# Kernel tuning notes

Hardware: AMD Instinct MI355X
Metric: run time of the kernel (lower is better)

Reference implementation:

```python
import jax, jax.numpy as jnp
import numpy as np

Z, K, H, Y = 128, 256, 512, 4  # z_size, key_size, hidden_size, y_dim


def setup_inputs() -> dict:
    key = jax.random.key(0)
    ks = jax.random.split(key, 8)
    B, T, P = 512, 32, 32
    s = lambda k, shape, sc: (jax.random.normal(k, shape, jnp.float32) * sc)
    return {
        "x_seq": jax.random.normal(ks[0], (B, T, P, P), jnp.float32),
        "W_enc": s(ks[1], (P * P, Z), 0.03),
        "gamma": jnp.ones((Z,), jnp.float32),
        "beta": jnp.zeros((Z,), jnp.float32),
        "W_ih": s(ks[2], (4 * H, K + 1), 0.05),
        "W_hh": s(ks[3], (4 * H, H), 0.04),
        "b_ih": jnp.zeros((4 * H,), jnp.float32),
        "b_hh": jnp.zeros((4 * H,), jnp.float32),
        "W_key": s(ks[4], (K, H), 0.06),
        "b_key": jnp.zeros((K,), jnp.float32),
        "W_g": s(ks[5], (1, H), 0.06),
        "b_g": jnp.zeros((1,), jnp.float32),
        "conf_gain": jnp.ones((1,), jnp.float32),
        "conf_bias": jnp.zeros((1,), jnp.float32),
        "W_y": s(ks[6], (Y, H), 0.06),
        "b_y": jnp.zeros((Y,), jnp.float32),
    }


def _lstm_cell(x, h, c, W_ih, W_hh, b_ih, b_hh):
    # PyTorch gate order: i, f, g, o
    gates = x @ W_ih.T + b_ih + h @ W_hh.T + b_hh
    i, f, g, o = jnp.split(gates, 4, axis=-1)
    c = jax.nn.sigmoid(f) * c + jax.nn.sigmoid(i) * jnp.tanh(g)
    h = jax.nn.sigmoid(o) * jnp.tanh(c)
    return h, c


def _forward(x_seq, W_enc, gamma, beta, W_ih, W_hh, b_ih, b_hh,
             W_key, b_key, W_g, b_g, conf_gain, conf_bias, W_y, b_y):
    B, T, P, _ = x_seq.shape
    # encoder: flatten -> linear to z_size (stand-in for Encoder_mlp)
    z = x_seq.reshape(B, T, P * P) @ W_enc  # [B, T, Z]
    # context norm over the sequence dim (single task segment)
    mu = z.mean(axis=1, keepdims=True)
    sig = jnp.sqrt(z.var(axis=1, keepdims=True) + 1e-8)
    z = (z - mu) / sig * gamma + beta

    M = T + 1  # T+1 steps; final step feeds a zero z_t
    z_pad = jnp.concatenate([z, jnp.zeros((B, 1, Z), z.dtype)], axis=1)  # [B, M, Z]

    h0 = jnp.zeros((B, H), z.dtype)
    c0 = jnp.zeros((B, H), z.dtype)
    kr0 = jnp.zeros((B, K + 1), z.dtype)
    Mk0 = jnp.zeros((B, M, K), z.dtype)
    Mv0 = jnp.zeros((B, M, Z), z.dtype)

    def step(carry, t):
        h, c, key_r, M_k, M_v = carry
        z_t = jax.lax.dynamic_index_in_dim(z_pad, t, axis=1, keepdims=False)  # [B, Z]
        h, c = _lstm_cell(key_r, h, c, W_ih, W_hh, b_ih, b_hh)
        key_w = jax.nn.relu(h @ W_key.T + b_key)          # [B, K]
        g = jax.nn.sigmoid(h @ W_g.T + b_g)               # [B, 1]
        y_lin = h @ W_y.T + b_y                            # [B, Y]
        # attention read over valid memory slots j < t
        scores = jnp.einsum('bz,bmz->bm', z_t, M_v)        # [B, M]
        valid = (jnp.arange(M) < t)[None, :]
        w_k = jax.nn.softmax(jnp.where(valid, scores, -1e9), axis=1)
        c_k = jax.nn.sigmoid(scores * conf_gain + conf_bias)
        kv = jnp.concatenate([M_k, c_k[..., None]], axis=2)  # [B, M, K+1]
        attn = g * jnp.einsum('bm,bmd->bd', w_k, kv)          # [B, K+1]
        key_r_new = jnp.where(t == 0, jnp.zeros_like(attn), attn)
        # append to memory at slot t
        M_k = jax.lax.dynamic_update_slice_in_dim(M_k, key_w[:, None, :], t, axis=1)
        M_v = jax.lax.dynamic_update_slice_in_dim(M_v, z_t[:, None, :], t, axis=1)
        return (h, c, key_r_new, M_k, M_v), y_lin

    _, ys = jax.lax.scan(step, (h0, c0, kr0, Mk0, Mv0), jnp.arange(M))
    return ys[-1]  # y_pred_linear from final step, [B, Y]


def reference(x_seq, W_enc, gamma, beta, W_ih, W_hh, b_ih, b_hh,
              W_key, b_key, W_g, b_g, conf_gain, conf_bias, W_y, b_y):
    y_pred_linear = _forward(x_seq, W_enc, gamma, beta, W_ih, W_hh, b_ih, b_hh,
                             W_key, b_key, W_g, b_g, conf_gain, conf_bias, W_y, b_y)
    y_pred = jnp.argmax(y_pred_linear, axis=1)
    return y_pred_linear, y_pred
```

## Files before the change

kernel.cpp:

```cpp
#include <hip/hip_runtime.h>
#include <math.h>

typedef unsigned short ushort;
typedef unsigned int uint;
typedef __bf16 bf16x8 __attribute__((ext_vector_type(8)));
typedef float f32x4 __attribute__((ext_vector_type(4)));

#define ZS    128
#define KS    256
#define HS    512
#define BATCH 512
#define TT    32
#define MM    33
#define NB    2304
#define KPAD  800
#define HOFF  272
#define LDA   800

static __device__ __forceinline__ float sigf(float x) { return 1.f / (1.f + expf(-x)); }
static __device__ __forceinline__ float bf2f(ushort u) { return __uint_as_float((uint)u << 16); }

__global__ void prep_w(const float* __restrict__ W_ih, const float* __restrict__ W_hh,
                       const float* __restrict__ W_key, const float* __restrict__ b_ih,
                       const float* __restrict__ b_hh, const float* __restrict__ b_key,
                       const float* __restrict__ W_enc,
                       ushort* __restrict__ Whi, ushort* __restrict__ Wlo,
                       ushort* __restrict__ Behi, ushort* __restrict__ Belo,
                       float* __restrict__ biasN)
{
    int idx = blockIdx.x * 256 + threadIdx.x;
    if (idx < NB) {
        float bv;
        if (idx < 2048) { int j = idx >> 2, gi = idx & 3, r = gi * 512 + j; bv = b_ih[r] + b_hh[r]; }
        else bv = b_key[idx - 2048];
        biasN[idx] = bv;
    }
    if (idx < NB * KPAD) {
        int n = idx / KPAD, k = idx - n * KPAD;
        float v = 0.f;
        if (n < 2048) {
            int j = n >> 2, gi = n & 3, r = gi * 512 + j;
            if (k < 257) v = W_ih[r * 257 + k];
            else if (k >= HOFF && k < HOFF + 512) v = W_hh[r * 512 + (k - HOFF)];
        } else {
            if (k >= HOFF && k < HOFF + 512) v = W_key[(n - 2048) * 512 + (k - HOFF)];
        }
        uint u = __float_as_uint(v);
        Whi[idx] = (ushort)(u >> 16);
        float lo = v - __uint_as_float(u & 0xFFFF0000u);
        Wlo[idx] = (ushort)(__float_as_uint(lo) >> 16);
    } else if (idx < NB * KPAD + 128 * 1024) {
        int e = idx - NB * KPAD;
        int n = e >> 10, k = e & 1023;
        float v = W_enc[k * 128 + n];
        uint u = __float_as_uint(v);
        Behi[e] = (ushort)(u >> 16);
        float lo = v - __uint_as_float(u & 0xFFFF0000u);
        Belo[e] = (ushort)(__float_as_uint(lo) >> 16);
    }
}

template<int BN, int MODE, bool PRESPLIT>
__global__ __launch_bounds__(256, 4)
void gemm_mfma(const float* __restrict__ A,
               const ushort* __restrict__ Ahi, const ushort* __restrict__ Alo, int lda,
               const ushort* __restrict__ Bhi, const ushort* __restrict__ Blo, int ldb,
               int nslice,
               float* __restrict__ out,
               ushort* __restrict__ outHi, ushort* __restrict__ outLo,
               const float* __restrict__ biasN,
               float* __restrict__ cst, float* __restrict__ Mk, int step)
{
    constexpr int NI = BN / 32;
    constexpr int AHI = 0, ALO = 32 * 40, BHI = 64 * 40, BLO = 64 * 40 + BN * 40;
    constexpr int BUF = 64 * 40 + 2 * BN * 40;
    __shared__ ushort lds[2 * BUF];

    const int tid = threadIdx.x;
    const int bx = blockIdx.x, by = blockIdx.y;
    const int row0 = by * 32, n0 = bx * BN;
    const int l = tid & 63, w = tid >> 6, wm = w >> 1, wn = w & 1;
    const int lm = l & 15, kg = (l >> 4) << 3;

    f32x4 acc[NI];
    const f32x4 zero4 = {0.f, 0.f, 0.f, 0.f};
#pragma unroll
    for (int ni = 0; ni < NI; ni++) acc[ni] = zero4;

    float4 avf;
    uint4 avu;
    uint4 bhv[BN / 64], blv[BN / 64];

    auto LOADG = [&](int s) {
        const int k0 = s * 32;
        if (PRESPLIT) {
            int idx = tid & 127, r = idx >> 2, c = (idx & 3) << 3;
            const ushort* src = (tid < 128) ? Ahi : Alo;
            avu = *(const uint4*)(src + (size_t)(row0 + r) * lda + k0 + c);
        } else {
            int r = tid >> 3, c = (tid & 7) << 2;
            avf = *(const float4*)(A + (size_t)(row0 + r) * lda + k0 + c);
        }
#pragma unroll
        for (int i = 0; i < BN / 64; i++) {
            int idx = tid + 256 * i, r = idx >> 2, c = (idx & 3) << 3;
            bhv[i] = *(const uint4*)(Bhi + (size_t)(n0 + r) * ldb + k0 + c);
            blv[i] = *(const uint4*)(Blo + (size_t)(n0 + r) * ldb + k0 + c);
        }
    };
    auto STORE = [&](int buf) {
        ushort* L = lds + buf * BUF;
        if (PRESPLIT) {
            int idx = tid & 127, r = idx >> 2, c = (idx & 3) << 3;
            *(uint4*)&L[(tid < 128 ? AHI : ALO) + r * 40 + c] = avu;
        } else {
            int r = tid >> 3, c = (tid & 7) << 2;
            uint u0 = __float_as_uint(avf.x), u1 = __float_as_uint(avf.y);
            uint u2 = __float_as_uint(avf.z), u3 = __float_as_uint(avf.w);
            uint hp0 = (u1 & 0xFFFF0000u) | (u0 >> 16);
            uint hp1 = (u3 & 0xFFFF0000u) | (u2 >> 16);
            float l0 = avf.x - __uint_as_float(u0 & 0xFFFF0000u);
            float l1 = avf.y - __uint_as_float(u1 & 0xFFFF0000u);
            float l2 = avf.z - __uint_as_float(u2 & 0xFFFF0000u);
            float l3 = avf.w - __uint_as_float(u3 & 0xFFFF0000u);
            uint lp0 = (__float_as_uint(l1) & 0xFFFF0000u) | (__float_as_uint(l0) >> 16);
            uint lp1 = (__float_as_uint(l3) & 0xFFFF0000u) | (__float_as_uint(l2) >> 16);
            *(uint2*)&L[AHI + r * 40 + c] = make_uint2(hp0, hp1);
            *(uint2*)&L[ALO + r * 40 + c] = make_uint2(lp0, lp1);
        }
#pragma unroll
        for (int i = 0; i < BN / 64; i++) {
            int idx = tid + 256 * i, r = idx >> 2, c = (idx & 3) << 3;
            *(uint4*)&L[BHI + r * 40 + c] = bhv[i];
            *(uint4*)&L[BLO + r * 40 + c] = blv[i];
        }
    };

    LOADG(0);
    STORE(0);
    for (int s = 0; s < nslice; s++) {
        if (s + 1 < nslice) LOADG(s + 1);
        __syncthreads();
        const ushort* L = lds + (s & 1) * BUF;
        bf16x8 ah, alv, bh[NI], bl[NI];
        {
            int r = wm * 16 + lm;
            ah  = *(const bf16x8*)&L[AHI + r * 40 + kg];
            alv = *(const bf16x8*)&L[ALO + r * 40 + kg];
        }
#pragma unroll
        for (int ni = 0; ni < NI; ni++) {
            int r = wn * (BN / 2) + ni * 16 + lm;
            bh[ni] = *(const bf16x8*)&L[BHI + r * 40 + kg];
            bl[ni] = *(const bf16x8*)&L[BLO + r * 40 + kg];
        }
#pragma unroll
        for (int ni = 0; ni < NI; ni++) {
            acc[ni] = __builtin_amdgcn_mfma_f32_16x16x32_bf16(ah,  bh[ni], acc[ni], 0, 0, 0);
            acc[ni] = __builtin_amdgcn_mfma_f32_16x16x32_bf16(ah,  bl[ni], acc[ni], 0, 0, 0);
            acc[ni] = __builtin_amdgcn_mfma_f32_16x16x32_bf16(alv, bh[ni], acc[ni], 0, 0, 0);
        }
        if (s + 1 < nslice) STORE((s + 1) & 1);
    }

    const int crow = (l >> 4) << 2;
    if (MODE == 0) {
#pragma unroll
        for (int ni = 0; ni < NI; ni++)
#pragma unroll
            for (int r = 0; r < 4; r++) {
                int m = row0 + wm * 16 + crow + r;
                int z = n0 + wn * (BN / 2) + ni * 16 + lm;
                out[(size_t)(m >> 5) * (MM * ZS) + (m & 31) * ZS + z] = acc[ni][r];
            }
    } else if (bx < 32) {
        __syncthreads();
        float* epi = (float*)lds;
        float* ew = epi + w * 544;
#pragma unroll
        for (int ni = 0; ni < NI; ni++)
#pragma unroll
            for (int r = 0; r < 4; r++) {
                int ml = crow + r, nl = ni * 16 + lm;
                ew[ml * 34 + nl] = acc[ni][r] + biasN[n0 + wn * 32 + nl];
            }
        __syncthreads();
        int row = tid >> 3, jj8 = tid & 7;
        int b = row0 + row;
        int j0 = bx * 16 + jj8 * 2;
        float2 cold = *(float2*)&cst[(size_t)b * HS + j0];
        float cc[2] = {cold.x, cold.y}, hv[2];
#pragma unroll
        for (int i = 0; i < 2; i++) {
            int jj = jj8 * 2 + i;
            float p[4];
#pragma unroll
            for (int g = 0; g < 4; g++) {
                int n = jj * 4 + g;
                int wv = (row >> 4) * 2 + (n >> 5);
                p[g] = epi[wv * 544 + (row & 15) * 34 + (n & 31)];
            }
            float ig = sigf(p[0]), fg = sigf(p[1]), gg = tanhf(p[2]), og = sigf(p[3]);
            float cn = fg * cc[i] + ig * gg;
            hv[i] = og * tanhf(cn);
            cc[i] = cn;
        }
        *(float2*)&cst[(size_t)b * HS + j0] = make_float2(cc[0], cc[1]);
        uint u0 = __float_as_uint(hv[0]), u1 = __float_as_uint(hv[1]);
        uint hp = (u1 & 0xFFFF0000u) | (u0 >> 16);
        float l0 = hv[0] - __uint_as_float(u0 & 0xFFFF0000u);
        float l1 = hv[1] - __uint_as_float(u1 & 0xFFFF0000u);
        uint lp = (__float_as_uint(l1) & 0xFFFF0000u) | (__float_as_uint(l0) >> 16);
        *(uint*)&outHi[(size_t)b * LDA + HOFF + j0] = hp;
        *(uint*)&outLo[(size_t)b * LDA + HOFF + j0] = lp;
    } else if (step >= 1) {
#pragma unroll
        for (int ni = 0; ni < NI; ni++)
#pragma unroll
            for (int r = 0; r < 4; r++) {
                int b = row0 + wm * 16 + crow + r;
                int cg = n0 + wn * 32 + ni * 16 + lm;
                float v = fmaxf(acc[ni][r] + biasN[cg], 0.f);
                Mk[((size_t)(step - 1) * BATCH + b) * KS + (cg - 2048)] = v;
            }
    }
}

__global__ void norm_k(float* __restrict__ z_pad, const float* __restrict__ gamma,
                       const float* __restrict__ beta)
{
    int b = blockIdx.x, zc = threadIdx.x;
    float* zb = z_pad + (size_t)b * (MM * ZS);
    float s = 0.f, s2 = 0.f;
    for (int t = 0; t < TT; t++) { float v = zb[t * ZS + zc]; s += v; s2 += v * v; }
    float mu = s * (1.f / 32.f);
    float var = s2 * (1.f / 32.f) - mu * mu;
    float rstd = 1.f / sqrtf(var + 1e-8f);
    float ga = gamma[zc], be = beta[zc];
    for (int t = 0; t < TT; t++) {
        float v = zb[t * ZS + zc];
        zb[t * ZS + zc] = (v - mu) * rstd * ga + be;
    }
    zb[TT * ZS + zc] = 0.f;
}

__global__ __launch_bounds__(256)
void scores_k(const float* __restrict__ z_pad, const float* __restrict__ cg_p,
              const float* __restrict__ cb_p, float* __restrict__ watt,
              float* __restrict__ wc)
{
    __shared__ float zs[MM * 129];
    int b = blockIdx.x, tid = threadIdx.x;
    const float* zb = z_pad + (size_t)b * (MM * ZS);
    for (int i = tid; i < MM * ZS; i += 256) {
        int m = i >> 7, k = i & 127;
        zs[m * 129 + k] = zb[i];
    }
    __syncthreads();
    float cg = cg_p[0], cb = cb_p[0];
    int wid = tid >> 6, lane = tid & 63;
    for (int t = 1 + wid; t <= 32; t += 4) {
        int m = lane;
        float s = -3.0e38f;
        if (m < t) {
            const float* zt = &zs[t * 129];
            const float* zm = &zs[m * 129];
            float acc = 0.f;
#pragma unroll 8
            for (int k = 0; k < ZS; k++) acc += zt[k] * zm[k];
            s = acc;
        }
        float mx = s;
        for (int off = 1; off < 64; off <<= 1) mx = fmaxf(mx, __shfl_xor(mx, off));
        float e = (m < t) ? expf(s - mx) : 0.f;
        float sum = e;
        for (int off = 1; off < 64; off <<= 1) sum += __shfl_xor(sum, off);
        float w = e / sum;
        if (m < t) watt[(b * MM + t) * MM + m] = w;
        float p = (m < t) ? w * sigf(s * cg + cb) : 0.f;
        for (int off = 1; off < 64; off <<= 1) p += __shfl_xor(p, off);
        if (lane == 0) wc[b * MM + t] = p;
    }
}

__global__ __launch_bounds__(256)
void post_k(ushort* __restrict__ inpHi, ushort* __restrict__ inpLo,
            const float* __restrict__ W_g, const float* __restrict__ b_g,
            const float* __restrict__ watt, const float* __restrict__ wc,
            const float* __restrict__ Mk, int t)
{
    __shared__ float red[256];
    __shared__ float wts[32];
    __shared__ float gsh;
    int b = blockIdx.x, tid = threadIdx.x;
    ushort* rHi = inpHi + (size_t)b * LDA;
    ushort* rLo = inpLo + (size_t)b * LDA;
    float h1 = bf2f(rHi[HOFF + tid]) + bf2f(rLo[HOFF + tid]);
    float h2 = bf2f(rHi[HOFF + 256 + tid]) + bf2f(rLo[HOFF + 256 + tid]);
    red[tid] = h1 * W_g[tid] + h2 * W_g[tid + 256];
    if (tid < t) wts[tid] = watt[(b * MM + t) * MM + tid];
    __syncthreads();
    for (int s = 128; s > 0; s >>= 1) {
        if (tid < s) red[tid] += red[tid + s];
        __syncthreads();
    }
    if (tid == 0) gsh = sigf(red[0] + b_g[0]);
    __syncthreads();
    float g = gsh;
    float acc = 0.f;
    for (int m = 0; m < t; m++)
        acc += wts[m] * Mk[((size_t)m * BATCH + b) * KS + tid];
    float v = g * acc;
    uint u = __float_as_uint(v);
    rHi[tid] = (ushort)(u >> 16);
    float lo = v - __uint_as_float(u & 0xFFFF0000u);
    rLo[tid] = (ushort)(__float_as_uint(lo) >> 16);
    if (tid == 0) {
        float vc = g * wc[b * MM + t];
        uint uc = __float_as_uint(vc);
        rHi[256] = (ushort)(uc >> 16);
        float lc = vc - __uint_as_float(uc & 0xFFFF0000u);
        rLo[256] = (ushort)(__float_as_uint(lc) >> 16);
    }
}

__global__ void y_k(const ushort* __restrict__ inpHi, const ushort* __restrict__ inpLo,
                    const float* __restrict__ W_y, const float* __restrict__ b_y,
                    float* __restrict__ out)
{
    int b = blockIdx.x, lane = threadIdx.x;
    const ushort* hHi = inpHi + (size_t)b * LDA + HOFF;
    const ushort* hLo = inpLo + (size_t)b * LDA + HOFF;
    float a0 = 0, a1 = 0, a2 = 0, a3 = 0;
    for (int r = 0; r < 8; r++) {
        int k = lane + r * 64;
        float hv = bf2f(hHi[k]) + bf2f(hLo[k]);
        a0 += hv * W_y[k];
        a1 += hv * W_y[512 + k];
        a2 += hv * W_y[1024 + k];
        a3 += hv * W_y[1536 + k];
    }
    for (int off = 32; off > 0; off >>= 1) {
        a0 += __shfl_xor(a0, off);
        a1 += __shfl_xor(a1, off);
        a2 += __shfl_xor(a2, off);
        a3 += __shfl_xor(a3, off);
    }
    if (lane == 0) {
        float y0 = a0 + b_y[0], y1 = a1 + b_y[1], y2 = a2 + b_y[2], y3 = a3 + b_y[3];
        out[b * 4 + 0] = y0; out[b * 4 + 1] = y1; out[b * 4 + 2] = y2; out[b * 4 + 3] = y3;
        int best = 0; float bv = y0;
        if (y1 > bv) { bv = y1; best = 1; }
        if (y2 > bv) { bv = y2; best = 2; }
        if (y3 > bv) { bv = y3; best = 3; }
        out[2048 + b] = (float)best;
    }
}

extern "C" void kernel_launch(void* const* d_in, const int* in_sizes, int n_in,
                              void* d_out, int out_size, void* d_ws, size_t ws_size,
                              hipStream_t stream)
{
    const float* x_seq = (const float*)d_in[0];
    const float* W_enc = (const float*)d_in[1];
    const float* gamma = (const float*)d_in[2];
    const float* beta  = (const float*)d_in[3];
    const float* W_ih  = (const float*)d_in[4];
    const float* W_hh  = (const float*)d_in[5];
    const float* b_ih  = (const float*)d_in[6];
    const float* b_hh  = (const float*)d_in[7];
    const float* W_key = (const float*)d_in[8];
    const float* b_key = (const float*)d_in[9];
    const float* W_g   = (const float*)d_in[10];
    const float* b_g   = (const float*)d_in[11];
    const float* cgain = (const float*)d_in[12];
    const float* cbias = (const float*)d_in[13];
    const float* W_y   = (const float*)d_in[14];
    const float* b_y   = (const float*)d_in[15];

    float* ws    = (float*)d_ws;
    float* z_pad = ws;
    float* watt  = z_pad + 2162688;
    float* wcv   = watt + 557568;
    float* Mk    = wcv + 16896;
    float* biasN = Mk + 4194304;
    float* cst   = biasN + 2304;
    ushort* inpHi0 = (ushort*)(cst + 262144);
    ushort* inpLo0 = inpHi0 + 409600;
    ushort* inpHi1 = inpLo0 + 409600;
    ushort* inpLo1 = inpHi1 + 409600;
    ushort* Whi  = inpLo1 + 409600;
    ushort* Wlo  = Whi + NB * KPAD;
    ushort* Behi = Wlo + NB * KPAD;
    ushort* Belo = Behi + 131072;

    hipMemsetAsync(cst, 0, 262144 * sizeof(float) + 4 * 409600 * sizeof(ushort), stream);

    prep_w<<<(NB * KPAD + 131072 + 255) / 256, 256, 0, stream>>>(
        W_ih, W_hh, W_key, b_ih, b_hh, b_key, W_enc, Whi, Wlo, Behi, Belo, biasN);

    gemm_mfma<128, 0, false><<<dim3(1, 512), 256, 0, stream>>>(
        x_seq, nullptr, nullptr, 1024, Behi, Belo, 1024, 32,
        z_pad, nullptr, nullptr, nullptr, nullptr, nullptr, 0);
    norm_k<<<512, 128, 0, stream>>>(z_pad, gamma, beta);
    scores_k<<<512, 256, 0, stream>>>(z_pad, cgain, cbias, watt, wcv);

    for (int t = 0; t <= 32; t++) {
        ushort* inHiC = (t & 1) ? inpHi1 : inpHi0;
        ushort* inLoC = (t & 1) ? inpLo1 : inpLo0;
        ushort* inHiN = (t & 1) ? inpHi0 : inpHi1;
        ushort* inLoN = (t & 1) ? inpLo0 : inpLo1;
        gemm_mfma<64, 1, true><<<dim3(36, 16), 256, 0, stream>>>(
            nullptr, inHiC, inLoC, LDA, Whi, Wlo, KPAD, 25,
            nullptr, inHiN, inLoN, biasN, cst, Mk, t);
        if (t >= 1 && t <= 31)
            post_k<<<512, 256, 0, stream>>>(inHiN, inLoN, W_g, b_g, watt, wcv, Mk, t);
    }
    y_k<<<512, 64, 0, stream>>>((0 ? inpHi0 : inpHi1), (0 ? inpLo0 : inpLo1),
                                W_y, b_y, (float*)d_out);
}
```

Baseline: 1.016 ms.

## Split encoder GEMM K-dimension, swizzle recurrent GEMM blocks, double-register prefetch

The encoder GEMM is split along K into two halves via blockIdx.z, with the second half written into the Mk scratch buffer and summed in norm_k. This doubles the block count to fill the GPU. The recurrent GEMM uses a 1D grid with an XCD-style swizzle of block indices to improve cache locality. The main loop is unrolled by two with two register prefetch sets so global loads are issued two slices ahead, and encoder launch bounds are relaxed to 3 blocks per SM. The cost is more registers and an extra partial-sum buffer round trip.

```diff
diff --git a/kernel.cpp b/kernel.cpp
--- a/kernel.cpp
+++ b/kernel.cpp
@@ -60,8 +60,54 @@
     }
 }
 
+#define LOADG_M(s, avf_, avu_, bhv_, blv_) do {                                   \
+    const int k0 = (s) * 32;                                                      \
+    if (PRESPLIT) {                                                               \
+        int idx = tid & 127, r = idx >> 2, c = (idx & 3) << 3;                    \
+        const ushort* srcp = (tid < 128) ? Ahi : Alo;                             \
+        avu_ = *(const uint4*)(srcp + (size_t)(row0 + r) * lda + k0 + c);         \
+    } else {                                                                      \
+        int r = tid >> 3, c = (tid & 7) << 2;                                     \
+        avf_ = *(const float4*)(A + (size_t)(row0 + r) * lda + k0 + c);           \
+    }                                                                             \
+    _Pragma("unroll")                                                             \
+    for (int i = 0; i < BN / 64; i++) {                                           \
+        int idx2 = tid + 256 * i, r2 = idx2 >> 2, c2 = (idx2 & 3) << 3;           \
+        bhv_[i] = *(const uint4*)(Bhi + (size_t)(n0 + r2) * ldb + k0 + c2);       \
+        blv_[i] = *(const uint4*)(Blo + (size_t)(n0 + r2) * ldb + k0 + c2);       \
+    }                                                                             \
+} while (0)
+
+#define STORE_M(buf, avf_, avu_, bhv_, blv_) do {                                 \
+    ushort* Lw = lds + (buf) * BUF;                                               \
+    if (PRESPLIT) {                                                               \
+        int idx = tid & 127, r = idx >> 2, c = (idx & 3) << 3;                    \
+        *(uint4*)&Lw[(tid < 128 ? AHI : ALO) + r * 40 + c] = avu_;                \
+    } else {                                                                     \
+        int r = tid >> 3, c = (tid & 7) << 2;                                    \
+        uint u0 = __float_as_uint(avf_.x), u1 = __float_as_uint(avf_.y);          \
+        uint u2 = __float_as_uint(avf_.z), u3 = __float_as_uint(avf_.w);          \
+        uint hp0 = (u1 & 0xFFFF0000u) | (u0 >> 16);                               \
+        uint hp1 = (u3 & 0xFFFF0000u) | (u2 >> 16);                               \
+        float l0 = avf_.x - __uint_as_float(u0 & 0xFFFF0000u);                    \
+        float l1 = avf_.y - __uint_as_float(u1 & 0xFFFF0000u);                    \
+        float l2 = avf_.z - __uint_as_float(u2 & 0xFFFF0000u);                    \
+        float l3 = avf_.w - __uint_as_float(u3 & 0xFFFF0000u);                    \
+        uint lp0 = (__float_as_uint(l1) & 0xFFFF0000u) | (__float_as_uint(l0) >> 16); \
+        uint lp1 = (__float_as_uint(l3) & 0xFFFF0000u) | (__float_as_uint(l2) >> 16); \
+        *(uint2*)&Lw[AHI + r * 40 + c] = make_uint2(hp0, hp1);                    \
+        *(uint2*)&Lw[ALO + r * 40 + c] = make_uint2(lp0, lp1);                    \
+    }                                                                             \
+    _Pragma("unroll")                                                             \
+    for (int i = 0; i < BN / 64; i++) {                                           \
+        int idx3 = tid + 256 * i, r3 = idx3 >> 2, c3 = (idx3 & 3) << 3;           \
+        *(uint4*)&Lw[BHI + r3 * 40 + c3] = bhv_[i];                               \
+        *(uint4*)&Lw[BLO + r3 * 40 + c3] = blv_[i];                               \
+    }                                                                             \
+} while (0)
+
 template<int BN, int MODE, bool PRESPLIT>
-__global__ __launch_bounds__(256, 4)
+__global__ __launch_bounds__(256, (MODE == 0) ? 3 : 4)
 void gemm_mfma(const float* __restrict__ A,
                const ushort* __restrict__ Ahi, const ushort* __restrict__ Alo, int lda,
                const ushort* __restrict__ Bhi, const ushort* __restrict__ Blo, int ldb,
@@ -77,7 +123,18 @@
     __shared__ ushort lds[2 * BUF];
 
     const int tid = threadIdx.x;
-    const int bx = blockIdx.x, by = blockIdx.y;
+    int bx, by;
+    if (MODE == 1) {
+        int wg = blockIdx.x;
+        int swz = (wg & 7) * 72 + (wg >> 3);
+        bx = swz >> 4; by = swz & 15;
+    } else {
+        bx = blockIdx.x; by = blockIdx.y;
+        A   += (size_t)blockIdx.z * 512;
+        Bhi += (size_t)blockIdx.z * 512;
+        Blo += (size_t)blockIdx.z * 512;
+        if (blockIdx.z) out = Mk;
+    }
     const int row0 = by * 32, n0 = bx * BN;
     const int l = tid & 63, w = tid >> 6, wm = w >> 1, wn = w & 1;
     const int lm = l & 15, kg = (l >> 4) << 3;
@@ -87,60 +144,11 @@
 #pragma unroll
     for (int ni = 0; ni < NI; ni++) acc[ni] = zero4;
 
-    float4 avf;
-    uint4 avu;
-    uint4 bhv[BN / 64], blv[BN / 64];
-
-    auto LOADG = [&](int s) {
-        const int k0 = s * 32;
-        if (PRESPLIT) {
-            int idx = tid & 127, r = idx >> 2, c = (idx & 3) << 3;
-            const ushort* src = (tid < 128) ? Ahi : Alo;
-            avu = *(const uint4*)(src + (size_t)(row0 + r) * lda + k0 + c);
-        } else {
-            int r = tid >> 3, c = (tid & 7) << 2;
-            avf = *(const float4*)(A + (size_t)(row0 + r) * lda + k0 + c);
-        }
-#pragma unroll
-        for (int i = 0; i < BN / 64; i++) {
-            int idx = tid + 256 * i, r = idx >> 2, c = (idx & 3) << 3;
-            bhv[i] = *(const uint4*)(Bhi + (size_t)(n0 + r) * ldb + k0 + c);
-            blv[i] = *(const uint4*)(Blo + (size_t)(n0 + r) * ldb + k0 + c);
-        }
-    };
-    auto STORE = [&](int buf) {
-        ushort* L = lds + buf * BUF;
-        if (PRESPLIT) {
-            int idx = tid & 127, r = idx >> 2, c = (idx & 3) << 3;
-            *(uint4*)&L[(tid < 128 ? AHI : ALO) + r * 40 + c] = avu;
-        } else {
-            int r = tid >> 3, c = (tid & 7) << 2;
-            uint u0 = __float_as_uint(avf.x), u1 = __float_as_uint(avf.y);
-            uint u2 = __float_as_uint(avf.z), u3 = __float_as_uint(avf.w);
-            uint hp0 = (u1 & 0xFFFF0000u) | (u0 >> 16);
-            uint hp1 = (u3 & 0xFFFF0000u) | (u2 >> 16);
-            float l0 = avf.x - __uint_as_float(u0 & 0xFFFF0000u);
-            float l1 = avf.y - __uint_as_float(u1 & 0xFFFF0000u);
-            float l2 = avf.z - __uint_as_float(u2 & 0xFFFF0000u);
-            float l3 = avf.w - __uint_as_float(u3 & 0xFFFF0000u);
-            uint lp0 = (__float_as_uint(l1) & 0xFFFF0000u) | (__float_as_uint(l0) >> 16);
-            uint lp1 = (__float_as_uint(l3) & 0xFFFF0000u) | (__float_as_uint(l2) >> 16);
-            *(uint2*)&L[AHI + r * 40 + c] = make_uint2(hp0, hp1);
-            *(uint2*)&L[ALO + r * 40 + c] = make_uint2(lp0, lp1);
-        }
-#pragma unroll
-        for (int i = 0; i < BN / 64; i++) {
-            int idx = tid + 256 * i, r = idx >> 2, c = (idx & 3) << 3;
-            *(uint4*)&L[BHI + r * 40 + c] = bhv[i];
-            *(uint4*)&L[BLO + r * 40 + c] = blv[i];
-        }
-    };
-
-    LOADG(0);
-    STORE(0);
-    for (int s = 0; s < nslice; s++) {
-        if (s + 1 < nslice) LOADG(s + 1);
-        __syncthreads();
+    float4 avf0, avf1;
+    uint4 avu0, avu1;
+    uint4 bhv0[BN / 64], blv0[BN / 64], bhv1[BN / 64], blv1[BN / 64];
+
+    auto COMPUTE = [&](int s) {
         const ushort* L = lds + (s & 1) * BUF;
         bf16x8 ah, alv, bh[NI], bl[NI];
         {
@@ -160,7 +168,22 @@
             acc[ni] = __builtin_amdgcn_mfma_f32_16x16x32_bf16(ah,  bl[ni], acc[ni], 0, 0, 0);
             acc[ni] = __builtin_amdgcn_mfma_f32_16x16x32_bf16(alv, bh[ni], acc[ni], 0, 0, 0);
         }
-        if (s + 1 < nslice) STORE((s + 1) & 1);
+    };
+
+    LOADG_M(0, avf0, avu0, bhv0, blv0);
+    STORE_M(0, avf0, avu0, bhv0, blv0);
+    if (nslice > 1) LOADG_M(1, avf1, avu1, bhv1, blv1);
+    for (int s = 0; s < nslice; s += 2) {
+        if (s + 2 < nslice) LOADG_M(s + 2, avf0, avu0, bhv0, blv0);
+        __syncthreads();
+        COMPUTE(s);
+        if (s + 1 < nslice) STORE_M((s + 1) & 1, avf1, avu1, bhv1, blv1);
+        if (s + 3 < nslice) LOADG_M(s + 3, avf1, avu1, bhv1, blv1);
+        __syncthreads();
+        if (s + 1 < nslice) {
+            COMPUTE(s + 1);
+            if (s + 2 < nslice) STORE_M((s + 2) & 1, avf0, avu0, bhv0, blv0);
+        }
     }
 
     const int crow = (l >> 4) << 2;
@@ -226,13 +249,21 @@
     }
 }
 
-__global__ void norm_k(float* __restrict__ z_pad, const float* __restrict__ gamma,
-                       const float* __restrict__ beta)
+#undef LOADG_M
+#undef STORE_M
+
+__global__ void norm_k(float* __restrict__ z_pad, const float* __restrict__ z2,
+                       const float* __restrict__ gamma, const float* __restrict__ beta)
 {
     int b = blockIdx.x, zc = threadIdx.x;
     float* zb = z_pad + (size_t)b * (MM * ZS);
+    const float* zb2 = z2 + (size_t)b * (MM * ZS);
     float s = 0.f, s2 = 0.f;
-    for (int t = 0; t < TT; t++) { float v = zb[t * ZS + zc]; s += v; s2 += v * v; }
+    for (int t = 0; t < TT; t++) {
+        float v = zb[t * ZS + zc] + zb2[t * ZS + zc];
+        zb[t * ZS + zc] = v;
+        s += v; s2 += v * v;
+    }
     float mu = s * (1.f / 32.f);
     float var = s2 * (1.f / 32.f) - mu * mu;
     float rstd = 1.f / sqrtf(var + 1e-8f);
@@ -399,10 +430,10 @@
     prep_w<<<(NB * KPAD + 131072 + 255) / 256, 256, 0, stream>>>(
         W_ih, W_hh, W_key, b_ih, b_hh, b_key, W_enc, Whi, Wlo, Behi, Belo, biasN);
 
-    gemm_mfma<128, 0, false><<<dim3(1, 512), 256, 0, stream>>>(
-        x_seq, nullptr, nullptr, 1024, Behi, Belo, 1024, 32,
-        z_pad, nullptr, nullptr, nullptr, nullptr, nullptr, 0);
-    norm_k<<<512, 128, 0, stream>>>(z_pad, gamma, beta);
+    gemm_mfma<128, 0, false><<<dim3(1, 512, 2), 256, 0, stream>>>(
+        x_seq, nullptr, nullptr, 1024, Behi, Belo, 1024, 16,
+        z_pad, nullptr, nullptr, nullptr, nullptr, Mk, 0);
+    norm_k<<<512, 128, 0, stream>>>(z_pad, Mk, gamma, beta);
     scores_k<<<512, 256, 0, stream>>>(z_pad, cgain, cbias, watt, wcv);
 
     for (int t = 0; t <= 32; t++) {
@@ -410,7 +441,7 @@
         ushort* inLoC = (t & 1) ? inpLo1 : inpLo0;
         ushort* inHiN = (t & 1) ? inpHi0 : inpHi1;
         ushort* inLoN = (t & 1) ? inpLo0 : inpLo1;
-        gemm_mfma<64, 1, true><<<dim3(36, 16), 256, 0, stream>>>(
+        gemm_mfma<64, 1, true><<<dim3(576), 256, 0, stream>>>(
             nullptr, inHiC, inLoC, LDA, Whi, Wlo, KPAD, 25,
             nullptr, inHiN, inLoN, biasN, cst, Mk, t);
         if (t >= 1 && t <= 31)
```

New measurement: 1.058 ms. 4.2% more time.

## Split recurrent GEMM along K into two partials and fuse cell with attention

Applied to the files above, without the earlier changes.

The per-step recurrent GEMM now runs as 1152 workgroups: the K dimension is split into two halves (13 and 12 slices), each writing a separate partial result to P0/P1. Workgroup indices are swizzled and the occupancy hint is raised. The fused LSTM epilogue and key ReLU are moved out of the GEMM into a new cell_k kernel that sums the partials, applies the gates, writes Mk, and also performs the post_k gate and attention work, reusing h from shared memory and the fresh key from registers. The aim is more parallelism in the latency-bound step GEMM, paid for by extra global traffic for the partials.

```diff
diff --git a/kernel.cpp b/kernel.cpp
--- a/kernel.cpp
+++ b/kernel.cpp
@@ -61,15 +61,13 @@
 }
 
 template<int BN, int MODE, bool PRESPLIT>
-__global__ __launch_bounds__(256, 4)
+__global__ __launch_bounds__(256, (MODE == 1) ? 5 : 4)
 void gemm_mfma(const float* __restrict__ A,
                const ushort* __restrict__ Ahi, const ushort* __restrict__ Alo, int lda,
                const ushort* __restrict__ Bhi, const ushort* __restrict__ Blo, int ldb,
                int nslice,
                float* __restrict__ out,
-               ushort* __restrict__ outHi, ushort* __restrict__ outLo,
-               const float* __restrict__ biasN,
-               float* __restrict__ cst, float* __restrict__ Mk, int step)
+               float* __restrict__ out2)
 {
     constexpr int NI = BN / 32;
     constexpr int AHI = 0, ALO = 32 * 40, BHI = 64 * 40, BLO = 64 * 40 + BN * 40;
@@ -77,7 +75,20 @@
     __shared__ ushort lds[2 * BUF];
 
     const int tid = threadIdx.x;
-    const int bx = blockIdx.x, by = blockIdx.y;
+    int bx, by, kb, kc;
+    if (MODE == 1) {
+        int wg = blockIdx.x;
+        int swz = (wg & 7) * 144 + (wg >> 3);
+        int zz = swz / 576;
+        int r  = swz - zz * 576;
+        bx = r >> 4; by = r & 15;
+        kb = zz ? 13 : 0;
+        kc = zz ? 12 : 13;
+        if (zz) out = out2;
+    } else {
+        bx = blockIdx.x; by = blockIdx.y;
+        kb = 0; kc = nslice;
+    }
     const int row0 = by * 32, n0 = bx * BN;
     const int l = tid & 63, w = tid >> 6, wm = w >> 1, wn = w & 1;
     const int lm = l & 15, kg = (l >> 4) << 3;
@@ -91,8 +102,8 @@
     uint4 avu;
     uint4 bhv[BN / 64], blv[BN / 64];
 
-    auto LOADG = [&](int s) {
-        const int k0 = s * 32;
+    auto LOADG = [&](int a) {
+        const int k0 = a * 32;
         if (PRESPLIT) {
             int idx = tid & 127, r = idx >> 2, c = (idx & 3) << 3;
             const ushort* src = (tid < 128) ? Ahi : Alo;
@@ -135,13 +146,8 @@
             *(uint4*)&L[BLO + r * 40 + c] = blv[i];
         }
     };
-
-    LOADG(0);
-    STORE(0);
-    for (int s = 0; s < nslice; s++) {
-        if (s + 1 < nslice) LOADG(s + 1);
-        __syncthreads();
-        const ushort* L = lds + (s & 1) * BUF;
+    auto COMPUTE = [&](int buf) {
+        const ushort* L = lds + buf * BUF;
         bf16x8 ah, alv, bh[NI], bl[NI];
         {
             int r = wm * 16 + lm;
@@ -160,7 +166,15 @@
             acc[ni] = __builtin_amdgcn_mfma_f32_16x16x32_bf16(ah,  bl[ni], acc[ni], 0, 0, 0);
             acc[ni] = __builtin_amdgcn_mfma_f32_16x16x32_bf16(alv, bh[ni], acc[ni], 0, 0, 0);
         }
-        if (s + 1 < nslice) STORE((s + 1) & 1);
+    };
+
+    LOADG(kb);
+    STORE(0);
+    for (int s = 0; s < kc; s++) {
+        if (s + 1 < kc) LOADG(kb + s + 1);
+        __syncthreads();
+        COMPUTE(s & 1);
+        if (s + 1 < kc) STORE((s + 1) & 1);
     }
 
     const int crow = (l >> 4) << 2;
@@ -173,56 +187,84 @@
                 int z = n0 + wn * (BN / 2) + ni * 16 + lm;
                 out[(size_t)(m >> 5) * (MM * ZS) + (m & 31) * ZS + z] = acc[ni][r];
             }
-    } else if (bx < 32) {
-        __syncthreads();
-        float* epi = (float*)lds;
-        float* ew = epi + w * 544;
-#pragma unroll
-        for (int ni = 0; ni < NI; ni++)
-#pragma unroll
-            for (int r = 0; r < 4; r++) {
-                int ml = crow + r, nl = ni * 16 + lm;
-                ew[ml * 34 + nl] = acc[ni][r] + biasN[n0 + wn * 32 + nl];
-            }
-        __syncthreads();
-        int row = tid >> 3, jj8 = tid & 7;
-        int b = row0 + row;
-        int j0 = bx * 16 + jj8 * 2;
-        float2 cold = *(float2*)&cst[(size_t)b * HS + j0];
-        float cc[2] = {cold.x, cold.y}, hv[2];
-#pragma unroll
-        for (int i = 0; i < 2; i++) {
-            int jj = jj8 * 2 + i;
-            float p[4];
-#pragma unroll
-            for (int g = 0; g < 4; g++) {
-                int n = jj * 4 + g;
-                int wv = (row >> 4) * 2 + (n >> 5);
-                p[g] = epi[wv * 544 + (row & 15) * 34 + (n & 31)];
-            }
-            float ig = sigf(p[0]), fg = sigf(p[1]), gg = tanhf(p[2]), og = sigf(p[3]);
-            float cn = fg * cc[i] + ig * gg;
-            hv[i] = og * tanhf(cn);
-            cc[i] = cn;
-        }
-        *(float2*)&cst[(size_t)b * HS + j0] = make_float2(cc[0], cc[1]);
-        uint u0 = __float_as_uint(hv[0]), u1 = __float_as_uint(hv[1]);
-        uint hp = (u1 & 0xFFFF0000u) | (u0 >> 16);
-        float l0 = hv[0] - __uint_as_float(u0 & 0xFFFF0000u);
-        float l1 = hv[1] - __uint_as_float(u1 & 0xFFFF0000u);
-        uint lp = (__float_as_uint(l1) & 0xFFFF0000u) | (__float_as_uint(l0) >> 16);
-        *(uint*)&outHi[(size_t)b * LDA + HOFF + j0] = hp;
-        *(uint*)&outLo[(size_t)b * LDA + HOFF + j0] = lp;
-    } else if (step >= 1) {
+    } else {
 #pragma unroll
         for (int ni = 0; ni < NI; ni++)
 #pragma unroll
             for (int r = 0; r < 4; r++) {
                 int b = row0 + wm * 16 + crow + r;
-                int cg = n0 + wn * 32 + ni * 16 + lm;
-                float v = fmaxf(acc[ni][r] + biasN[cg], 0.f);
-                Mk[((size_t)(step - 1) * BATCH + b) * KS + (cg - 2048)] = v;
+                int n = n0 + wn * (BN / 2) + ni * 16 + lm;
+                out[(size_t)b * NB + n] = acc[ni][r];
             }
+    }
+}
+
+__global__ __launch_bounds__(256)
+void cell_k(const float* __restrict__ P0, const float* __restrict__ P1,
+            const float* __restrict__ biasN, float* __restrict__ cst,
+            ushort* __restrict__ outHi, ushort* __restrict__ outLo,
+            float* __restrict__ Mk,
+            const float* __restrict__ W_g, const float* __restrict__ b_g,
+            const float* __restrict__ watt, const float* __restrict__ wc,
+            int t)
+{
+    __shared__ float hsh[512];
+    __shared__ float red[256];
+    __shared__ float wts[32];
+    __shared__ float gsh;
+    int b = blockIdx.x, tid = threadIdx.x;
+    const float* p0 = P0 + (size_t)b * NB;
+    const float* p1 = P1 + (size_t)b * NB;
+    ushort* rHi = outHi + (size_t)b * LDA;
+    ushort* rLo = outLo + (size_t)b * LDA;
+#pragma unroll
+    for (int u = 0; u < 2; u++) {
+        int j = tid + u * 256;
+        float4 a  = *(const float4*)(p0 + 4 * j);
+        float4 c4 = *(const float4*)(p1 + 4 * j);
+        float4 bb = *(const float4*)(biasN + 4 * j);
+        float gi = a.x + c4.x + bb.x;
+        float gf = a.y + c4.y + bb.y;
+        float gg = a.z + c4.z + bb.z;
+        float go = a.w + c4.w + bb.w;
+        float iv = sigf(gi), fv = sigf(gf), gv = tanhf(gg), ov = sigf(go);
+        float cn = fv * cst[(size_t)b * HS + j] + iv * gv;
+        float hv = ov * tanhf(cn);
+        cst[(size_t)b * HS + j] = cn;
+        hsh[j] = hv;
+        uint uu = __float_as_uint(hv);
+        rHi[HOFF + j] = (ushort)(uu >> 16);
+        float lo = hv - __uint_as_float(uu & 0xFFFF0000u);
+        rLo[HOFF + j] = (ushort)(__float_as_uint(lo) >> 16);
+    }
+    float kv = fmaxf(p0[2048 + tid] + p1[2048 + tid] + biasN[2048 + tid], 0.f);
+    if (t >= 1) Mk[((size_t)(t - 1) * BATCH + b) * KS + tid] = kv;
+    if (t < 1 || t > 31) return;
+    if (tid < t) wts[tid] = watt[(b * MM + t) * MM + tid];
+    __syncthreads();
+    red[tid] = hsh[tid] * W_g[tid] + hsh[tid + 256] * W_g[tid + 256];
+    __syncthreads();
+    for (int s = 128; s > 0; s >>= 1) {
+        if (tid < s) red[tid] += red[tid + s];
+        __syncthreads();
+    }
+    if (tid == 0) gsh = sigf(red[0] + b_g[0]);
+    __syncthreads();
+    float g = gsh;
+    float acc = wts[t - 1] * kv;
+    for (int m = 0; m < t - 1; m++)
+        acc += wts[m] * Mk[((size_t)m * BATCH + b) * KS + tid];
+    float v = g * acc;
+    uint u2 = __float_as_uint(v);
+    rHi[tid] = (ushort)(u2 >> 16);
+    float lo2 = v - __uint_as_float(u2 & 0xFFFF0000u);
+    rLo[tid] = (ushort)(__float_as_uint(lo2) >> 16);
+    if (tid == 0) {
+        float vc = g * wc[b * MM + t];
+        uint uc = __float_as_uint(vc);
+        rHi[256] = (ushort)(uc >> 16);
+        float lc = vc - __uint_as_float(uc & 0xFFFF0000u);
+        rLo[256] = (ushort)(__float_as_uint(lc) >> 16);
     }
 }
 
@@ -280,47 +322,6 @@
         float p = (m < t) ? w * sigf(s * cg + cb) : 0.f;
         for (int off = 1; off < 64; off <<= 1) p += __shfl_xor(p, off);
         if (lane == 0) wc[b * MM + t] = p;
-    }
-}
-
-__global__ __launch_bounds__(256)
-void post_k(ushort* __restrict__ inpHi, ushort* __restrict__ inpLo,
-            const float* __restrict__ W_g, const float* __restrict__ b_g,
-            const float* __restrict__ watt, const float* __restrict__ wc,
-            const float* __restrict__ Mk, int t)
-{
-    __shared__ float red[256];
-    __shared__ float wts[32];
-    __shared__ float gsh;
-    int b = blockIdx.x, tid = threadIdx.x;
-    ushort* rHi = inpHi + (size_t)b * LDA;
-    ushort* rLo = inpLo + (size_t)b * LDA;
-    float h1 = bf2f(rHi[HOFF + tid]) + bf2f(rLo[HOFF + tid]);
-    float h2 = bf2f(rHi[HOFF + 256 + tid]) + bf2f(rLo[HOFF + 256 + tid]);
-    red[tid] = h1 * W_g[tid] + h2 * W_g[tid + 256];
-    if (tid < t) wts[tid] = watt[(b * MM + t) * MM + tid];
-    __syncthreads();
-    for (int s = 128; s > 0; s >>= 1) {
-        if (tid < s) red[tid] += red[tid + s];
-        __syncthreads();
-    }
-    if (tid == 0) gsh = sigf(red[0] + b_g[0]);
-    __syncthreads();
-    float g = gsh;
-    float acc = 0.f;
-    for (int m = 0; m < t; m++)
-        acc += wts[m] * Mk[((size_t)m * BATCH + b) * KS + tid];
-    float v = g * acc;
-    uint u = __float_as_uint(v);
-    rHi[tid] = (ushort)(u >> 16);
-    float lo = v - __uint_as_float(u & 0xFFFF0000u);
-    rLo[tid] = (ushort)(__float_as_uint(lo) >> 16);
-    if (tid == 0) {
-        float vc = g * wc[b * MM + t];
-        uint uc = __float_as_uint(vc);
-        rHi[256] = (ushort)(uc >> 16);
-        float lc = vc - __uint_as_float(uc & 0xFFFF0000u);
-        rLo[256] = (ushort)(__float_as_uint(lc) >> 16);
     }
 }
 
@@ -393,6 +394,8 @@
     ushort* Wlo  = Whi + NB * KPAD;
     ushort* Behi = Wlo + NB * KPAD;
     ushort* Belo = Behi + 131072;
+    float* P0 = (float*)(Belo + 131072);
+    float* P1 = P0 + (size_t)BATCH * NB;
 
     hipMemsetAsync(cst, 0, 262144 * sizeof(float) + 4 * 409600 * sizeof(ushort), stream);
 
@@ -401,7 +404,7 @@
 
     gemm_mfma<128, 0, false><<<dim3(1, 512), 256, 0, stream>>>(
         x_seq, nullptr, nullptr, 1024, Behi, Belo, 1024, 32,
-        z_pad, nullptr, nullptr, nullptr, nullptr, nullptr, 0);
+        z_pad, nullptr);
     norm_k<<<512, 128, 0, stream>>>(z_pad, gamma, beta);
     scores_k<<<512, 256, 0, stream>>>(z_pad, cgain, cbias, watt, wcv);
 
@@ -410,12 +413,11 @@
         ushort* inLoC = (t & 1) ? inpLo1 : inpLo0;
         ushort* inHiN = (t & 1) ? inpHi0 : inpHi1;
         ushort* inLoN = (t & 1) ? inpLo0 : inpLo1;
-        gemm_mfma<64, 1, true><<<dim3(36, 16), 256, 0, stream>>>(
+        gemm_mfma<64, 1, true><<<dim3(1152), 256, 0, stream>>>(
             nullptr, inHiC, inLoC, LDA, Whi, Wlo, KPAD, 25,
-            nullptr, inHiN, inLoN, biasN, cst, Mk, t);
-        if (t >= 1 && t <= 31)
-            post_k<<<512, 256, 0, stream>>>(inHiN, inLoN, W_g, b_g, watt, wcv, Mk, t);
-    }
-    y_k<<<512, 64, 0, stream>>>((0 ? inpHi0 : inpHi1), (0 ? inpLo0 : inpLo1),
-                                W_y, b_y, (float*)d_out);
-}
+            P0, P1);
+        cell_k<<<512, 256, 0, stream>>>(P0, P1, biasN, cst, inHiN, inLoN,
+                                        Mk, W_g, b_g, watt, wcv, t);
+    }
+    y_k<<<512, 64, 0, stream>>>(inpHi1, inpLo1, W_y, b_y, (float*)d_out);
+}
```

After: 1.011 ms. Within noise of the previous version (-0.4%).
